# Optimization experiments

Measured on AMD Instinct MI355X. Metric: run time of the kernel, lower is better.

The kernel has to match this reference:

```python
import jax, jax.numpy as jnp
import numpy as np
from jax import lax

ITER_ = 3
SMOOTH = 1e-05

B, C, D, H, W = 2, 3, 128, 160, 160


def _maxpool_axis(x, axis):
    # 3-wide max pool along one axis, stride 1, pad 1 (torch pads with -inf for max pool)
    win = [1] * x.ndim
    win[axis] = 3
    pad = [(0, 0)] * x.ndim
    pad[axis] = (1, 1)
    return lax.reduce_window(x, -jnp.inf, lax.max, tuple(win), (1,) * x.ndim, tuple(pad))


def _soft_erode(x):
    # min over axis-aligned erosions (erode = -maxpool(-x))
    nx = -x
    p1 = -_maxpool_axis(nx, 2)
    p2 = -_maxpool_axis(nx, 3)
    p3 = -_maxpool_axis(nx, 4)
    return jnp.minimum(jnp.minimum(p1, p2), p3)


def _soft_dilate(x):
    pad = ((0, 0), (0, 0), (1, 1), (1, 1), (1, 1))
    return lax.reduce_window(x, -jnp.inf, lax.max, (1, 1, 3, 3, 3), (1,) * 5, pad)


def _soft_open(x):
    return _soft_dilate(_soft_erode(x))


def _soft_skel(x):
    skel = jax.nn.relu(x - _soft_open(x))
    x_work = x
    for _ in range(ITER_):
        x_work = _soft_erode(x_work)
        delta = jax.nn.relu(x_work - _soft_open(x_work))
        skel = skel + jax.nn.relu(delta - skel * delta)
    return skel


def setup_inputs() -> dict:
    key = jax.random.key(0)
    k1, k2 = jax.random.split(key)
    net_output = jax.random.uniform(k1, (B, C, D, H, W), dtype=jnp.float32)
    target = jax.random.randint(k2, (B, 1, D, H, W), 0, C, dtype=jnp.int64)
    return {"net_output": net_output, "target": target}


def reference(net_output, target):
    num_classes = net_output.shape[1]
    labels = jnp.clip(target[:, 0], 0, num_classes - 1)
    target_1h = jax.nn.one_hot(labels, num_classes, dtype=net_output.dtype)  # [B,D,H,W,C]
    target_1h = jnp.moveaxis(target_1h, -1, 1)  # [B,C,D,H,W]

    # include_background=False, num_classes > 1 -> drop background channel
    pred = net_output[:, 1:]
    gt = target_1h[:, 1:]

    skel_pred = _soft_skel(pred)
    skel_gt = _soft_skel(gt)

    dims = (2, 3, 4)
    tprec = (jnp.sum(skel_pred * gt, dims) + SMOOTH) / (jnp.sum(skel_pred, dims) + SMOOTH)
    tsens = (jnp.sum(skel_gt * pred, dims) + SMOOTH) / (jnp.sum(skel_gt, dims) + SMOOTH)
    cl_dice = (2.0 * tprec * tsens + SMOOTH) / (tprec + tsens + SMOOTH)
    return 1.0 - jnp.mean(cl_dice)
```

## Files before the change

kernel.cpp:

```cpp
#include <hip/hip_runtime.h>
#include <math.h>

#define D_ 128
#define H_ 160
#define W_ 160
#define HW_ (H_ * W_)
#define V_ (D_ * H_ * W_)
#define SMOOTHF 1e-5

#define R_ 16
#define TY 10
#define ZC 32
#define COLS 40
#define NT 640
#define LROW 41
#define NYT 16
#define NZC 4
#define NTB (NYT * NZC)

__device__ __forceinline__ float max3f(float a, float b, float c) { return fmaxf(fmaxf(a, b), c); }
__device__ __forceinline__ float min3f(float a, float b, float c) { return fminf(fminf(a, b), c); }
__device__ __forceinline__ float4 f4min(float4 a, float4 b) {
    return make_float4(fminf(a.x,b.x), fminf(a.y,b.y), fminf(a.z,b.z), fminf(a.w,b.w));
}
__device__ __forceinline__ float4 f4max(float4 a, float4 b) {
    return make_float4(fmaxf(a.x,b.x), fmaxf(a.y,b.y), fmaxf(a.z,b.z), fmaxf(a.w,b.w));
}
__device__ __forceinline__ float4 min3x(float l, float4 c, float r) {
    return make_float4(min3f(l,c.x,c.y), min3f(c.x,c.y,c.z), min3f(c.y,c.z,c.w), min3f(c.z,c.w,r));
}
__device__ __forceinline__ float4 max3x(float l, float4 c, float r) {
    return make_float4(max3f(l,c.x,c.y), max3f(c.x,c.y,c.z), max3f(c.y,c.z,c.w), max3f(c.z,c.w,r));
}
__device__ __forceinline__ float4 relu4sub(float4 a, float4 b) {
    return make_float4(fmaxf(a.x-b.x,0.f), fmaxf(a.y-b.y,0.f), fmaxf(a.z-b.z,0.f), fmaxf(a.w-b.w,0.f));
}
__device__ __forceinline__ float4 skel_upd(float4 s, float4 d) {
    return make_float4(s.x + fmaxf(d.x - s.x*d.x, 0.f), s.y + fmaxf(d.y - s.y*d.y, 0.f),
                       s.z + fmaxf(d.z - s.z*d.z, 0.f), s.w + fmaxf(d.w - s.w*d.w, 0.f));
}

__device__ __forceinline__ void block_sync_lds() {
    asm volatile("s_waitcnt lgkmcnt(0)" ::: "memory");
    __builtin_amdgcn_s_barrier();
    asm volatile("" ::: "memory");
}

__device__ __forceinline__ float4 load_src4(const float* __restrict__ net,
                                            const int* __restrict__ tgt,
                                            int i, long p) {
    if (i < 4) {
        int b = i >> 1, c = (i & 1) + 1;
        return *(const float4*)(net + (long)(b * 3 + c) * V_ + p);
    } else {
        int j = i - 4;
        int b = j >> 1, c = (j & 1) + 1;
        int4 t = *(const int4*)(tgt + (long)b * V_ + p);
        float4 o;
        int tx = t.x < 0 ? 0 : (t.x > 2 ? 2 : t.x);
        int ty = t.y < 0 ? 0 : (t.y > 2 ? 2 : t.y);
        int tz = t.z < 0 ? 0 : (t.z > 2 ? 2 : t.z);
        int tw = t.w < 0 ? 0 : (t.w > 2 ? 2 : t.w);
        o.x = (tx == c) ? 1.0f : 0.0f;
        o.y = (ty == c) ? 1.0f : 0.0f;
        o.z = (tz == c) ? 1.0f : 0.0f;
        o.w = (tw == c) ? 1.0f : 0.0f;
        return o;
    }
}

template <int VAR>
__global__ __launch_bounds__(NT, 4) void fused_pair(
    const float* __restrict__ net, const int* __restrict__ tgt, int i0,
    const float* __restrict__ e_in, float* __restrict__ e_out,
    float* __restrict__ skel, float* __restrict__ partials) {

    __shared__ float4 Pb[2][R_ * LROW];
    __shared__ float4 E1b[2][R_ * LROW];
    __shared__ float4 E2b[2][R_ * LROW];
    __shared__ float smr[NT / 64][2];

    const int j = blockIdx.y, i = i0 + j;
    const int bx = blockIdx.x;
    const int y0 = (bx % NYT) * TY;
    const int z0 = (bx / NYT) * ZC;
    const int tid = threadIdx.x;
    const int r  = tid / COLS;
    const int x4 = tid - r * COLS;
    const int y  = y0 - 3 + r;
    const bool yok  = (y >= 0 && y < H_);
    const bool ymok = (y - 1 >= 0 && y - 1 < H_);
    const bool ypok = (y + 1 >= 0 && y + 1 < H_);
    const int rm = (r > 0) ? r - 1 : 0;
    const int rp = (r < R_ - 1) ? r + 1 : R_ - 1;
    const int xm = (x4 > 0) ? x4 - 1 : 0;
    const int xp = (x4 < COLS - 1) ? x4 + 1 : COLS - 1;
    const bool fxm = (x4 > 0), fxp = (x4 < COLS - 1);
    const bool rout = (r >= 3 && r < 3 + TY);
    const long colbase = (long)(yok ? y : 0) * W_ + x4 * 4;

    const float* ein_v = (VAR == 1) ? e_in + (long)j * V_ : nullptr;
    float* eout_v = (VAR == 0) ? e_out + (long)j * V_ : nullptr;
    float* skel_v = skel + (long)j * V_;
    const int ipart = (i < 4) ? (i + 4) : (i - 4);

    const float4 INF4  = make_float4( INFINITY,  INFINITY,  INFINITY,  INFINITY);
    const float4 NINF4 = make_float4(-INFINITY, -INFINITY, -INFINITY, -INFINITY);

    float4 p1 = INF4, p2 = INF4;
    float4 b1 = NINF4, b2 = NINF4, b3 = NINF4;
    float4 c1 = NINF4;
    float4 x1a = NINF4, x1b = NINF4, x1c = NINF4;
    float4 x2a = NINF4, x2b = NINF4;
    float acc0 = 0.f, acc1 = 0.f;

    float4 a_inflight = INF4;
    {
        const int sf = z0 - 3;
        if (sf >= 0 && sf < D_ && yok) {
            long p = (long)sf * HW_ + colbase;
            a_inflight = (VAR == 0) ? load_src4(net, tgt, i, p)
                                    : *(const float4*)(ein_v + p);
        }
    }

    for (int s = z0 - 3; s <= z0 + ZC + 3; ++s) {
        float4 anew = a_inflight;
        if (s <= z0 + ZC + 2) {
            Pb[s & 1][r * LROW + x4] = anew;
        }
        {
            const int sn = s + 1;
            float4 v = INF4;
            if (sn <= z0 + ZC + 2 && sn >= 0 && sn < D_ && yok) {
                long p = (long)sn * HW_ + colbase;
                v = (VAR == 0) ? load_src4(net, tgt, i, p)
                               : *(const float4*)(ein_v + p);
            }
            a_inflight = v;
        }
        const int zo = s - 4;
        const bool outok = (zo >= z0 && zo < z0 + ZC && rout);
        const long po = (long)(outok ? zo : z0) * HW_ + colbase;
        float4 cin_o = INF4, psk_o = INF4, ppr_o = INF4;
        if (outok) {
            if (VAR == 0) {
                cin_o = load_src4(net, tgt, i, po);
            } else {
                cin_o = *(const float4*)(ein_v + po);
                psk_o = *(const float4*)(skel_v + po);
                ppr_o = load_src4(net, tgt, ipart, po);
            }
        }

        float4 fe1 = NINF4;
        if (s >= z0 - 1 && s <= z0 + ZC + 2) {
            const int z1 = s - 1;
            const bool z1ok = (z1 >= 0 && z1 < D_);
            const float4* Pp = Pb[z1 & 1];
            float4 up = Pp[rm * LROW + x4];
            float4 dn = Pp[rp * LROW + x4];
            float lf = Pp[r * LROW + xm].w;
            float rt = Pp[r * LROW + xp].x;
            if (!ymok) up = INF4;
            if (!ypok) dn = INF4;
            if (!fxm) lf = INFINITY;
            if (!fxp) rt = INFINITY;
            float4 e = f4min(f4min(min3x(lf, p1, rt), f4min(up, dn)), f4min(p2, anew));
            if (!z1ok || !yok) e = NINF4;
            fe1 = e;
            E1b[z1 & 1][r * LROW + x4] = e;
        }

        float4 fe2 = NINF4, f1 = NINF4;
        if (s >= z0 + 1 && s <= z0 + ZC + 2) {
            const int z2 = s - 2;
            const bool z2ok = (z2 >= 0 && z2 < D_);
            const float4* Ep = E1b[z2 & 1];
            float4 n01 = Ep[rm * LROW + x4];
            float4 n21 = Ep[rp * LROW + x4];
            float4 c = b1;
            float l0 = fxm ? Ep[rm * LROW + xm].w : -INFINITY;
            float r0 = fxp ? Ep[rm * LROW + xp].x : -INFINITY;
            float l1 = fxm ? Ep[r  * LROW + xm].w : -INFINITY;
            float r1 = fxp ? Ep[r  * LROW + xp].x : -INFINITY;
            float l2 = fxm ? Ep[rp * LROW + xm].w : -INFINITY;
            float r2 = fxp ? Ep[rp * LROW + xp].x : -INFINITY;
            {
                float4 up = ymok ? n01 : INF4;
                float4 dn = ypok ? n21 : INF4;
                float lf = fxm ? l1 : INFINITY;
                float rt = fxp ? r1 : INFINITY;
                float4 zu = (z2 >= 1)     ? b2  : INF4;
                float4 zd = (z2 + 1 < D_) ? fe1 : INF4;
                float4 e = f4min(f4min(min3x(lf, c, rt), f4min(up, dn)), f4min(zu, zd));
                if (!z2ok || !yok) e = NINF4;
                fe2 = e;
            }
            {
                float4 m = f4max(f4max(max3x(l0, n01, r0), max3x(l1, c, r1)), max3x(l2, n21, r2));
                if (!z2ok) m = NINF4;
                f1 = m;
            }
            E2b[z2 & 1][r * LROW + x4] = fe2;
            if (VAR == 0 && z2 >= z0 && z2 < z0 + ZC && rout) {
                *(float4*)(eout_v + (long)z2 * HW_ + colbase) = fe2;
            }
        }

        float4 f2 = NINF4;
        if (s >= z0 + 2) {
            const int z3 = s - 3;
            const float4* Eq = E2b[z3 & 1];
            float4 m01 = Eq[rm * LROW + x4];
            float4 m21 = Eq[rp * LROW + x4];
            float l0 = fxm ? Eq[rm * LROW + xm].w : -INFINITY;
            float r0 = fxp ? Eq[rm * LROW + xp].x : -INFINITY;
            float l1 = fxm ? Eq[r  * LROW + xm].w : -INFINITY;
            float r1 = fxp ? Eq[r  * LROW + xp].x : -INFINITY;
            float l2 = fxm ? Eq[rp * LROW + xm].w : -INFINITY;
            float r2 = fxp ? Eq[rp * LROW + xp].x : -INFINITY;
            f2 = f4max(f4max(max3x(l0, m01, r0), max3x(l1, c1, r1)), max3x(l2, m21, r2));
        }

        if (outok) {
            float4 dil1 = f4max(f4max(x1a, x1b), x1c);
            float4 dil2 = f4max(f4max(x2a, x2b), f2);
            float4 ce1 = b3;
            if (VAR == 0) {
                float4 s0 = relu4sub(cin_o, dil1);
                float4 d1 = relu4sub(ce1, dil2);
                *(float4*)(skel_v + po) = skel_upd(s0, d1);
            } else {
                float4 d2 = relu4sub(cin_o, dil1);
                float4 sp = skel_upd(psk_o, d2);
                float4 d3 = relu4sub(ce1, dil2);
                float4 fin = skel_upd(sp, d3);
                acc0 += fin.x * ppr_o.x + fin.y * ppr_o.y + fin.z * ppr_o.z + fin.w * ppr_o.w;
                acc1 += fin.x + fin.y + fin.z + fin.w;
            }
        }

        p2 = p1; p1 = anew;
        b3 = b2; b2 = b1; b1 = fe1;
        c1 = fe2;
        x1a = x1b; x1b = x1c; x1c = f1;
        x2a = x2b; x2b = f2;

        block_sync_lds();
    }

    if (VAR == 1) {
        #pragma unroll
        for (int off = 32; off > 0; off >>= 1) {
            acc0 += __shfl_down(acc0, off);
            acc1 += __shfl_down(acc1, off);
        }
        int wid = tid >> 6, lane = tid & 63;
        __syncthreads();
        if (lane == 0) { smr[wid][0] = acc0; smr[wid][1] = acc1; }
        __syncthreads();
        if (tid == 0) {
            float t0 = 0.f, t1 = 0.f;
            #pragma unroll
            for (int w = 0; w < NT / 64; ++w) { t0 += smr[w][0]; t1 += smr[w][1]; }
            long base = ((long)i * NTB + bx) * 2;
            partials[base + 0] = t0;
            partials[base + 1] = t1;
        }
    }
}

__global__ void reduce_partials_kernel(const float* __restrict__ partials,
                                       int i0,
                                       double* __restrict__ sums) {
    int i = i0 + blockIdx.x;
    int t = threadIdx.x;
    long base = ((long)i * NTB + t) * 2;
    double v0 = (double)partials[base + 0];
    double v1 = (double)partials[base + 1];
    #pragma unroll
    for (int off = 32; off > 0; off >>= 1) {
        v0 += __shfl_down(v0, off);
        v1 += __shfl_down(v1, off);
    }
    if (t == 0) {
        sums[2 * i + 0] = v0;
        sums[2 * i + 1] = v1;
    }
}

__global__ void finalize_kernel(const double* __restrict__ sums,
                                float* __restrict__ out) {
    if (threadIdx.x == 0 && blockIdx.x == 0) {
        double acc = 0.0;
        #pragma unroll
        for (int i = 0; i < 4; ++i) {
            double tprec = (sums[2 * i + 0] + SMOOTHF) / (sums[2 * i + 1] + SMOOTHF);
            double tsens = (sums[2 * (i + 4) + 0] + SMOOTHF) / (sums[2 * (i + 4) + 1] + SMOOTHF);
            double cl = (2.0 * tprec * tsens + SMOOTHF) / (tprec + tsens + SMOOTHF);
            acc += cl;
        }
        out[0] = (float)(1.0 - acc * 0.25);
    }
}

extern "C" void kernel_launch(void* const* d_in, const int* in_sizes, int n_in,
                              void* d_out, int out_size, void* d_ws, size_t ws_size,
                              hipStream_t stream) {
    const float* net = (const float*)d_in[0];
    const int* tgt = (const int*)d_in[1];
    float* out = (float*)d_out;

    char* ws = (char*)d_ws;
    double* sums = (double*)ws;
    float* partials = (float*)(ws + 256);
    size_t head = 256 + (size_t)8 * NTB * 2 * sizeof(float);
    head = (head + 255) & ~(size_t)255;
    float* base = (float*)(ws + head);

    size_t perVol = (size_t)2 * V_ * sizeof(float);
    int G = 1;
    if (ws_size >= head + perVol * 8) G = 8;
    else if (ws_size >= head + perVol * 4) G = 4;
    else if (ws_size >= head + perVol * 2) G = 2;

    dim3 blk(NT);
    dim3 grd(NTB, G);

    for (int i0 = 0; i0 < 8; i0 += G) {
        float* SKEL = base;
        float* E2buf = base + (size_t)G * V_;

        fused_pair<0><<<grd, blk, 0, stream>>>(net, tgt, i0, nullptr, E2buf, SKEL, nullptr);
        fused_pair<1><<<grd, blk, 0, stream>>>(net, tgt, i0, E2buf, nullptr, SKEL, partials);

        reduce_partials_kernel<<<G, 64, 0, stream>>>(partials, i0, sums);
    }

    finalize_kernel<<<1, 64, 0, stream>>>(sums, out);
}
```

Measured before the change: 299.2 us.

## Halve z-chunk depth for more blocks and single-buffer LDS with two barriers

Halves the z-chunk per block and doubles the number of z-chunks, so the grid has twice as many blocks. The double-buffered LDS planes become single-buffered, with writes moved to the end of each step between two barriers. The partial-sum reducer is widened to 128 threads with a two-wave shared-memory combine to cover the larger block count. The costs are more halo recomputation per output plane (7 extra planes over 16 instead of 32), an extra barrier per z-step, and more redundant halo loads.

```diff
diff --git a/kernel.cpp b/kernel.cpp
--- a/kernel.cpp
+++ b/kernel.cpp
@@ -10,12 +10,12 @@
 
 #define R_ 16
 #define TY 10
-#define ZC 32
+#define ZC 16
 #define COLS 40
 #define NT 640
 #define LROW 41
 #define NYT 16
-#define NZC 4
+#define NZC 8
 #define NTB (NYT * NZC)
 
 __device__ __forceinline__ float max3f(float a, float b, float c) { return fmaxf(fmaxf(a, b), c); }
@@ -75,9 +75,9 @@
     const float* __restrict__ e_in, float* __restrict__ e_out,
     float* __restrict__ skel, float* __restrict__ partials) {
 
-    __shared__ float4 Pb[2][R_ * LROW];
-    __shared__ float4 E1b[2][R_ * LROW];
-    __shared__ float4 E2b[2][R_ * LROW];
+    __shared__ float4 Pb[R_ * LROW];
+    __shared__ float4 E1b[R_ * LROW];
+    __shared__ float4 E2b[R_ * LROW];
     __shared__ float smr[NT / 64][2];
 
     const int j = blockIdx.y, i = i0 + j;
@@ -126,9 +126,6 @@
 
     for (int s = z0 - 3; s <= z0 + ZC + 3; ++s) {
         float4 anew = a_inflight;
-        if (s <= z0 + ZC + 2) {
-            Pb[s & 1][r * LROW + x4] = anew;
-        }
         {
             const int sn = s + 1;
             float4 v = INF4;
@@ -142,7 +139,7 @@
         const int zo = s - 4;
         const bool outok = (zo >= z0 && zo < z0 + ZC && rout);
         const long po = (long)(outok ? zo : z0) * HW_ + colbase;
-        float4 cin_o = INF4, psk_o = INF4, ppr_o = INF4;
+        float4 cin_o = INF4, psk_o = make_float4(0,0,0,0), ppr_o = make_float4(0,0,0,0);
         if (outok) {
             if (VAR == 0) {
                 cin_o = load_src4(net, tgt, i, po);
@@ -153,15 +150,15 @@
             }
         }
 
+
         float4 fe1 = NINF4;
         if (s >= z0 - 1 && s <= z0 + ZC + 2) {
             const int z1 = s - 1;
             const bool z1ok = (z1 >= 0 && z1 < D_);
-            const float4* Pp = Pb[z1 & 1];
-            float4 up = Pp[rm * LROW + x4];
-            float4 dn = Pp[rp * LROW + x4];
-            float lf = Pp[r * LROW + xm].w;
-            float rt = Pp[r * LROW + xp].x;
+            float4 up = Pb[rm * LROW + x4];
+            float4 dn = Pb[rp * LROW + x4];
+            float lf = Pb[r * LROW + xm].w;
+            float rt = Pb[r * LROW + xp].x;
             if (!ymok) up = INF4;
             if (!ypok) dn = INF4;
             if (!fxm) lf = INFINITY;
@@ -169,23 +166,21 @@
             float4 e = f4min(f4min(min3x(lf, p1, rt), f4min(up, dn)), f4min(p2, anew));
             if (!z1ok || !yok) e = NINF4;
             fe1 = e;
-            E1b[z1 & 1][r * LROW + x4] = e;
         }
 
         float4 fe2 = NINF4, f1 = NINF4;
         if (s >= z0 + 1 && s <= z0 + ZC + 2) {
             const int z2 = s - 2;
             const bool z2ok = (z2 >= 0 && z2 < D_);
-            const float4* Ep = E1b[z2 & 1];
-            float4 n01 = Ep[rm * LROW + x4];
-            float4 n21 = Ep[rp * LROW + x4];
+            float4 n01 = E1b[rm * LROW + x4];
+            float4 n21 = E1b[rp * LROW + x4];
             float4 c = b1;
-            float l0 = fxm ? Ep[rm * LROW + xm].w : -INFINITY;
-            float r0 = fxp ? Ep[rm * LROW + xp].x : -INFINITY;
-            float l1 = fxm ? Ep[r  * LROW + xm].w : -INFINITY;
-            float r1 = fxp ? Ep[r  * LROW + xp].x : -INFINITY;
-            float l2 = fxm ? Ep[rp * LROW + xm].w : -INFINITY;
-            float r2 = fxp ? Ep[rp * LROW + xp].x : -INFINITY;
+            float l0 = fxm ? E1b[rm * LROW + xm].w : -INFINITY;
+            float r0 = fxp ? E1b[rm * LROW + xp].x : -INFINITY;
+            float l1 = fxm ? E1b[r  * LROW + xm].w : -INFINITY;
+            float r1 = fxp ? E1b[r  * LROW + xp].x : -INFINITY;
+            float l2 = fxm ? E1b[rp * LROW + xm].w : -INFINITY;
+            float r2 = fxp ? E1b[rp * LROW + xp].x : -INFINITY;
             {
                 float4 up = ymok ? n01 : INF4;
                 float4 dn = ypok ? n21 : INF4;
@@ -202,7 +197,6 @@
                 if (!z2ok) m = NINF4;
                 f1 = m;
             }
-            E2b[z2 & 1][r * LROW + x4] = fe2;
             if (VAR == 0 && z2 >= z0 && z2 < z0 + ZC && rout) {
                 *(float4*)(eout_v + (long)z2 * HW_ + colbase) = fe2;
             }
@@ -210,16 +204,14 @@
 
         float4 f2 = NINF4;
         if (s >= z0 + 2) {
-            const int z3 = s - 3;
-            const float4* Eq = E2b[z3 & 1];
-            float4 m01 = Eq[rm * LROW + x4];
-            float4 m21 = Eq[rp * LROW + x4];
-            float l0 = fxm ? Eq[rm * LROW + xm].w : -INFINITY;
-            float r0 = fxp ? Eq[rm * LROW + xp].x : -INFINITY;
-            float l1 = fxm ? Eq[r  * LROW + xm].w : -INFINITY;
-            float r1 = fxp ? Eq[r  * LROW + xp].x : -INFINITY;
-            float l2 = fxm ? Eq[rp * LROW + xm].w : -INFINITY;
-            float r2 = fxp ? Eq[rp * LROW + xp].x : -INFINITY;
+            float4 m01 = E2b[rm * LROW + x4];
+            float4 m21 = E2b[rp * LROW + x4];
+            float l0 = fxm ? E2b[rm * LROW + xm].w : -INFINITY;
+            float r0 = fxp ? E2b[rm * LROW + xp].x : -INFINITY;
+            float l1 = fxm ? E2b[r  * LROW + xm].w : -INFINITY;
+            float r1 = fxp ? E2b[r  * LROW + xp].x : -INFINITY;
+            float l2 = fxm ? E2b[rp * LROW + xm].w : -INFINITY;
+            float r2 = fxp ? E2b[rp * LROW + xp].x : -INFINITY;
             f2 = f4max(f4max(max3x(l0, m01, r0), max3x(l1, c1, r1)), max3x(l2, m21, r2));
         }
 
@@ -241,13 +233,19 @@
             }
         }
 
+        block_sync_lds();
+
+        Pb[r * LROW + x4]  = anew;
+        E1b[r * LROW + x4] = fe1;
+        E2b[r * LROW + x4] = fe2;
+
+        block_sync_lds();
+
         p2 = p1; p1 = anew;
         b3 = b2; b2 = b1; b1 = fe1;
         c1 = fe2;
         x1a = x1b; x1b = x1c; x1c = f1;
         x2a = x2b; x2b = f2;
-
-        block_sync_lds();
     }
 
     if (VAR == 1) {
@@ -284,9 +282,13 @@
         v0 += __shfl_down(v0, off);
         v1 += __shfl_down(v1, off);
     }
+    __shared__ double sm[2][2];
+    int wid = t >> 6, lane = t & 63;
+    if (lane == 0) { sm[wid][0] = v0; sm[wid][1] = v1; }
+    __syncthreads();
     if (t == 0) {
-        sums[2 * i + 0] = v0;
-        sums[2 * i + 1] = v1;
+        sums[2 * i + 0] = sm[0][0] + sm[1][0];
+        sums[2 * i + 1] = sm[0][1] + sm[1][1];
     }
 }
 
@@ -335,7 +337,7 @@
         fused_pair<0><<<grd, blk, 0, stream>>>(net, tgt, i0, nullptr, E2buf, SKEL, nullptr);
         fused_pair<1><<<grd, blk, 0, stream>>>(net, tgt, i0, E2buf, nullptr, SKEL, partials);
 
-        reduce_partials_kernel<<<G, 64, 0, stream>>>(partials, i0, sums);
+        reduce_partials_kernel<<<G, 128, 0, stream>>>(partials, i0, sums);
     }
 
     finalize_kernel<<<1, 64, 0, stream>>>(sums, out);
```

After: 333.6 us. +11.5%, slower.
